# Kernel optimization log

Measured on AMD Instinct MI355X. Metric: run time of the kernel, lower is better.

The kernel has to match this reference:

```python
import jax, jax.numpy as jnp
import numpy as np

N_NODES = 50000
N_EDGES = 1600000
D_FEAT = 32


def setup_inputs() -> dict:
    key = jax.random.key(0)
    k1, k2, k3, k4 = jax.random.split(key, 4)
    node_feat = jax.random.normal(k1, (N_NODES, D_FEAT), dtype=jnp.float32)
    edge_feat = jax.random.normal(k2, (N_EDGES, D_FEAT), dtype=jnp.float32)
    eps = jnp.zeros((1,), dtype=jnp.float32)  # learnable eps, init 0
    src = jax.random.randint(k3, (N_EDGES,), 0, N_NODES, dtype=jnp.int64)
    dst = jax.random.randint(k4, (N_EDGES,), 0, N_NODES, dtype=jnp.int64)
    return {"node_feat": node_feat, "edge_feat": edge_feat, "eps": eps,
            "src": src, "dst": dst}


def reference(node_feat, edge_feat, eps, src, dst):
    # message: relu(h_src + h_edge) per edge  [E, D]
    m = jax.nn.relu(node_feat[src] + edge_feat)
    # sum-aggregate messages into destination nodes  [N, D]
    neigh = jax.ops.segment_sum(m, dst, num_segments=node_feat.shape[0])
    # eps-scaled residual
    return (1.0 + eps[0]) * node_feat + neigh
```

## Files before the change

### kernel.cpp

```cpp
#include <hip/hip_runtime.h>

#define N_NODES 50000
#define N_EDGES 1600000
#define D_FEAT 32
#define SCAN_THREADS 1024

#define WS_CNT   0
#define WS_OFF   (N_NODES)
#define WS_RANK  (2 * N_NODES)
#define WS_MSG   (2 * N_NODES + N_EDGES)

static __device__ __forceinline__ unsigned short f2bf(float f) {
    unsigned u = __float_as_uint(f);
    unsigned r = (u + 0x7FFFu + ((u >> 16) & 1u)) >> 16;
    return (unsigned short)r;
}
static __device__ __forceinline__ float bf2f(unsigned short h) {
    return __uint_as_float(((unsigned)h) << 16);
}

__global__ void hist_rank(const int* __restrict__ dst,
                          int* __restrict__ cnt,
                          int* __restrict__ rank) {
    int e = blockIdx.x * blockDim.x + threadIdx.x;
    if (e < N_EDGES) rank[e] = atomicAdd(&cnt[dst[e]], 1);
}

__global__ void scan_all(const int* __restrict__ cnt, int* __restrict__ off) {
    __shared__ int part[SCAN_THREADS];
    const int PER = (N_NODES + SCAN_THREADS - 1) / SCAN_THREADS;
    int t = threadIdx.x;
    int base = t * PER;
    int s = 0;
    for (int i = 0; i < PER; ++i) {
        int idx = base + i;
        if (idx < N_NODES) s += cnt[idx];
    }
    part[t] = s;
    __syncthreads();
    for (int o = 1; o < SCAN_THREADS; o <<= 1) {
        int v = (t >= o) ? part[t - o] : 0;
        __syncthreads();
        part[t] += v;
        __syncthreads();
    }
    int run = (t > 0) ? part[t - 1] : 0;
    for (int i = 0; i < PER; ++i) {
        int idx = base + i;
        if (idx < N_NODES) { off[idx] = run; run += cnt[idx]; }
    }
}

__global__ void build_msg_bf16(const float* __restrict__ node_feat,
                               const float* __restrict__ edge_feat,
                               const int* __restrict__ src,
                               const int* __restrict__ dst,
                               const int* __restrict__ off,
                               const int* __restrict__ rank,
                               unsigned int* __restrict__ msg) {
    int t = blockIdx.x * blockDim.x + threadIdx.x;
    int e = t >> 3;
    int g = t & 7;
    if (e >= N_EDGES) return;

    int d = dst[e];
    int pos = off[d] + rank[e];
    int s = src[e];

    float4 ef = ((const float4*)edge_feat)[(size_t)e * 8 + g];
    float4 nf = ((const float4*)node_feat)[s * 8 + g];
    float m0 = fmaxf(nf.x + ef.x, 0.f);
    float m1 = fmaxf(nf.y + ef.y, 0.f);
    float m2 = fmaxf(nf.z + ef.z, 0.f);
    float m3 = fmaxf(nf.w + ef.w, 0.f);

    uint2 packed;
    packed.x = (unsigned)f2bf(m0) | ((unsigned)f2bf(m1) << 16);
    packed.y = (unsigned)f2bf(m2) | ((unsigned)f2bf(m3) << 16);
    ((uint2*)msg)[(size_t)pos * 8 + g] = packed;
}

__global__ void reduce_msgs(const float* __restrict__ node_feat,
                            const float* __restrict__ eps,
                            const int* __restrict__ off,
                            const int* __restrict__ cnt,
                            const unsigned int* __restrict__ msg,
                            float* __restrict__ out) {
    int t = blockIdx.x * blockDim.x + threadIdx.x;
    int n = t >> 3;
    int g = t & 7;
    if (n >= N_NODES) return;

    int start = off[n];
    int c = cnt[n];

    float4 acc = make_float4(0.f, 0.f, 0.f, 0.f);
    for (int i = 0; i < c; ++i) {
        uint2 m = ((const uint2*)msg)[(size_t)(start + i) * 8 + g];
        acc.x += bf2f((unsigned short)(m.x & 0xFFFF));
        acc.y += bf2f((unsigned short)(m.x >> 16));
        acc.z += bf2f((unsigned short)(m.y & 0xFFFF));
        acc.w += bf2f((unsigned short)(m.y >> 16));
    }

    float scale = 1.0f + eps[0];
    float4 h = ((const float4*)node_feat)[n * 8 + g];
    float4 o;
    o.x = scale * h.x + acc.x;
    o.y = scale * h.y + acc.y;
    o.z = scale * h.z + acc.z;
    o.w = scale * h.w + acc.w;
    ((float4*)out)[n * 8 + g] = o;
}


__global__ void fb_init_out(const float* __restrict__ node_feat,
                            const float* __restrict__ eps,
                            float* __restrict__ out) {
    int i = blockIdx.x * blockDim.x + threadIdx.x;
    const int n4 = N_NODES * D_FEAT / 4;
    float scale = 1.0f + eps[0];
    if (i < n4) {
        float4 v = ((const float4*)node_feat)[i];
        v.x *= scale; v.y *= scale; v.z *= scale; v.w *= scale;
        ((float4*)out)[i] = v;
    }
}

__global__ void fb_scatter(const float* __restrict__ node_feat,
                           const float* __restrict__ edge_feat,
                           const int* __restrict__ src,
                           const int* __restrict__ dst,
                           float* __restrict__ out) {
    int t = blockIdx.x * blockDim.x + threadIdx.x;
    int e = t >> 3;
    int g = t & 7;
    if (e >= N_EDGES) return;
    int s = src[e];
    int d = dst[e];
    float4 nf = ((const float4*)node_feat)[s * 8 + g];
    float4 ef = ((const float4*)edge_feat)[(size_t)e * 8 + g];
    float* op = out + (size_t)d * D_FEAT + g * 4;
    unsafeAtomicAdd(op + 0, fmaxf(nf.x + ef.x, 0.f));
    unsafeAtomicAdd(op + 1, fmaxf(nf.y + ef.y, 0.f));
    unsafeAtomicAdd(op + 2, fmaxf(nf.z + ef.z, 0.f));
    unsafeAtomicAdd(op + 3, fmaxf(nf.w + ef.w, 0.f));
}

extern "C" void kernel_launch(void* const* d_in, const int* in_sizes, int n_in,
                              void* d_out, int out_size, void* d_ws, size_t ws_size,
                              hipStream_t stream) {
    const float* node_feat = (const float*)d_in[0];
    const float* edge_feat = (const float*)d_in[1];
    const float* eps       = (const float*)d_in[2];
    const int*   src       = (const int*)d_in[3];
    const int*   dst       = (const int*)d_in[4];
    float* out = (float*)d_out;

    const int B = 256;
    const size_t need = (size_t)WS_MSG * sizeof(int) + (size_t)N_EDGES * 64;

    if (ws_size < need) {
        int n4 = N_NODES * D_FEAT / 4;
        fb_init_out<<<(n4 + B - 1) / B, B, 0, stream>>>(node_feat, eps, out);
        long long total = (long long)N_EDGES * 8;
        fb_scatter<<<(int)((total + B - 1) / B), B, 0, stream>>>(
            node_feat, edge_feat, src, dst, out);
        return;
    }

    int* ws = (int*)d_ws;
    int*          cnt  = ws + WS_CNT;
    int*          off  = ws + WS_OFF;
    int*          rank = ws + WS_RANK;
    unsigned int* msg  = (unsigned int*)(ws + WS_MSG);

    hipMemsetAsync(cnt, 0, N_NODES * sizeof(int), stream);

    hist_rank<<<(N_EDGES + B - 1) / B, B, 0, stream>>>(dst, cnt, rank);
    scan_all<<<1, SCAN_THREADS, 0, stream>>>(cnt, off);

    long long etotal = (long long)N_EDGES * 8;
    build_msg_bf16<<<(int)((etotal + B - 1) / B), B, 0, stream>>>(
        node_feat, edge_feat, src, dst, off, rank, msg);

    long long ntotal = (long long)N_NODES * 8;
    reduce_msgs<<<(int)((ntotal + B - 1) / B), B, 0, stream>>>(
        node_feat, eps, off, cnt, msg, out);
}
```

Measured before the change: 522.6 us.

## Sort edge index pairs instead of bf16 messages and gather in reduce

Replaces the materialized bf16 message buffer with a CSR-ordered list of (edge id, src) pairs, and moves the relu(node+edge) computation into the reduce kernel. The reduce now assigns one wavefront per node, with 8 sub-groups striding over incoming edges, and combines them with xor shuffles. This removes the bf16 round-trip write and read of the per-edge messages and the precision loss that came with it. In exchange the edge_feat reads become random gathers by edge id instead of sequential reads, and one 64-lane wave per node may leave lanes idle, since nodes average about 32 in-edges.

```diff
diff --git a/kernel.cpp b/kernel.cpp
--- a/kernel.cpp
+++ b/kernel.cpp
@@ -8,16 +8,7 @@
 #define WS_CNT   0
 #define WS_OFF   (N_NODES)
 #define WS_RANK  (2 * N_NODES)
-#define WS_MSG   (2 * N_NODES + N_EDGES)
-
-static __device__ __forceinline__ unsigned short f2bf(float f) {
-    unsigned u = __float_as_uint(f);
-    unsigned r = (u + 0x7FFFu + ((u >> 16) & 1u)) >> 16;
-    return (unsigned short)r;
-}
-static __device__ __forceinline__ float bf2f(unsigned short h) {
-    return __uint_as_float(((unsigned)h) << 16);
-}
+#define WS_PAIRS (2 * N_NODES + N_EDGES)
 
 __global__ void hist_rank(const int* __restrict__ dst,
                           int* __restrict__ cnt,
@@ -51,66 +42,62 @@
     }
 }
 
-__global__ void build_msg_bf16(const float* __restrict__ node_feat,
-                               const float* __restrict__ edge_feat,
-                               const int* __restrict__ src,
-                               const int* __restrict__ dst,
-                               const int* __restrict__ off,
-                               const int* __restrict__ rank,
-                               unsigned int* __restrict__ msg) {
-    int t = blockIdx.x * blockDim.x + threadIdx.x;
-    int e = t >> 3;
-    int g = t & 7;
+__global__ void scatter_pairs(const int* __restrict__ src,
+                              const int* __restrict__ dst,
+                              const int* __restrict__ off,
+                              const int* __restrict__ rank,
+                              int2* __restrict__ pairs) {
+    int e = blockIdx.x * blockDim.x + threadIdx.x;
     if (e >= N_EDGES) return;
-
-    int d = dst[e];
-    int pos = off[d] + rank[e];
-    int s = src[e];
-
-    float4 ef = ((const float4*)edge_feat)[(size_t)e * 8 + g];
-    float4 nf = ((const float4*)node_feat)[s * 8 + g];
-    float m0 = fmaxf(nf.x + ef.x, 0.f);
-    float m1 = fmaxf(nf.y + ef.y, 0.f);
-    float m2 = fmaxf(nf.z + ef.z, 0.f);
-    float m3 = fmaxf(nf.w + ef.w, 0.f);
-
-    uint2 packed;
-    packed.x = (unsigned)f2bf(m0) | ((unsigned)f2bf(m1) << 16);
-    packed.y = (unsigned)f2bf(m2) | ((unsigned)f2bf(m3) << 16);
-    ((uint2*)msg)[(size_t)pos * 8 + g] = packed;
+    int p = off[dst[e]] + rank[e];
+    pairs[p] = make_int2(e, src[e]);
 }
 
-__global__ void reduce_msgs(const float* __restrict__ node_feat,
-                            const float* __restrict__ eps,
-                            const int* __restrict__ off,
-                            const int* __restrict__ cnt,
-                            const unsigned int* __restrict__ msg,
-                            float* __restrict__ out) {
-    int t = blockIdx.x * blockDim.x + threadIdx.x;
-    int n = t >> 3;
-    int g = t & 7;
-    if (n >= N_NODES) return;
+__global__ void reduce_gather(const float* __restrict__ node_feat,
+                              const float* __restrict__ edge_feat,
+                              const float* __restrict__ eps,
+                              const int* __restrict__ off,
+                              const int* __restrict__ cnt,
+                              const int2* __restrict__ pairs,
+                              float* __restrict__ out) {
+    int wave = (blockIdx.x * blockDim.x + threadIdx.x) >> 6;
+    int lane = threadIdx.x & 63;
+    if (wave >= N_NODES) return;
+    int n = wave;
+    int g = lane & 7;
+    int sub = lane >> 3;
 
     int start = off[n];
     int c = cnt[n];
 
     float4 acc = make_float4(0.f, 0.f, 0.f, 0.f);
-    for (int i = 0; i < c; ++i) {
-        uint2 m = ((const uint2*)msg)[(size_t)(start + i) * 8 + g];
-        acc.x += bf2f((unsigned short)(m.x & 0xFFFF));
-        acc.y += bf2f((unsigned short)(m.x >> 16));
-        acc.z += bf2f((unsigned short)(m.y & 0xFFFF));
-        acc.w += bf2f((unsigned short)(m.y >> 16));
+    for (int i = sub; i < c; i += 8) {
+        int2 pr = pairs[start + i];
+        float4 ef = ((const float4*)edge_feat)[(size_t)pr.x * 8 + g];
+        float4 nf = ((const float4*)node_feat)[pr.y * 8 + g];
+        acc.x += fmaxf(nf.x + ef.x, 0.f);
+        acc.y += fmaxf(nf.y + ef.y, 0.f);
+        acc.z += fmaxf(nf.z + ef.z, 0.f);
+        acc.w += fmaxf(nf.w + ef.w, 0.f);
     }
 
-    float scale = 1.0f + eps[0];
-    float4 h = ((const float4*)node_feat)[n * 8 + g];
-    float4 o;
-    o.x = scale * h.x + acc.x;
-    o.y = scale * h.y + acc.y;
-    o.z = scale * h.z + acc.z;
-    o.w = scale * h.w + acc.w;
-    ((float4*)out)[n * 8 + g] = o;
+    for (int m = 8; m < 64; m <<= 1) {
+        acc.x += __shfl_xor(acc.x, m);
+        acc.y += __shfl_xor(acc.y, m);
+        acc.z += __shfl_xor(acc.z, m);
+        acc.w += __shfl_xor(acc.w, m);
+    }
+
+    if (sub == 0) {
+        float scale = 1.0f + eps[0];
+        float4 h = ((const float4*)node_feat)[n * 8 + g];
+        float4 o;
+        o.x = scale * h.x + acc.x;
+        o.y = scale * h.y + acc.y;
+        o.z = scale * h.z + acc.z;
+        o.w = scale * h.w + acc.w;
+        ((float4*)out)[n * 8 + g] = o;
+    }
 }
 
 
@@ -158,7 +145,7 @@
     float* out = (float*)d_out;
 
     const int B = 256;
-    const size_t need = (size_t)WS_MSG * sizeof(int) + (size_t)N_EDGES * 64;
+    const size_t need = (size_t)WS_PAIRS * sizeof(int) + (size_t)N_EDGES * sizeof(int2);
 
     if (ws_size < need) {
         int n4 = N_NODES * D_FEAT / 4;
@@ -169,22 +156,19 @@
         return;
     }
 
-    int* ws = (int*)d_ws;
-    int*          cnt  = ws + WS_CNT;
-    int*          off  = ws + WS_OFF;
-    int*          rank = ws + WS_RANK;
-    unsigned int* msg  = (unsigned int*)(ws + WS_MSG);
+    int*  ws    = (int*)d_ws;
+    int*  cnt   = ws + WS_CNT;
+    int*  off   = ws + WS_OFF;
+    int*  rank  = ws + WS_RANK;
+    int2* pairs = (int2*)(ws + WS_PAIRS);
 
     hipMemsetAsync(cnt, 0, N_NODES * sizeof(int), stream);
 
     hist_rank<<<(N_EDGES + B - 1) / B, B, 0, stream>>>(dst, cnt, rank);
     scan_all<<<1, SCAN_THREADS, 0, stream>>>(cnt, off);
+    scatter_pairs<<<(N_EDGES + B - 1) / B, B, 0, stream>>>(src, dst, off, rank, pairs);
 
-    long long etotal = (long long)N_EDGES * 8;
-    build_msg_bf16<<<(int)((etotal + B - 1) / B), B, 0, stream>>>(
-        node_feat, edge_feat, src, dst, off, rank, msg);
-
-    long long ntotal = (long long)N_NODES * 8;
-    reduce_msgs<<<(int)((ntotal + B - 1) / B), B, 0, stream>>>(
-        node_feat, eps, off, cnt, msg, out);
+    long long rthreads = (long long)N_NODES * 64;
+    reduce_gather<<<(int)((rthreads + B - 1) / B), B, 0, stream>>>(
+        node_feat, edge_feat, eps, off, cnt, pairs, out);
 }
```

New measurement: 513.1 us. Within noise of the previous version (-1.8%).
